# Performance work log

Measured on AMD Instinct MI355X. Metric: run time of the kernel, lower is better.

The kernel has to match this reference:

```python
import jax, jax.numpy as jnp
import numpy as np

B, S, DM = 2, 2048, 1024
H, D = 16, 64  # num_heads, head_dim
EPS = 1e-5


def setup_inputs() -> dict:
    key = jax.random.key(0)
    ks = jax.random.split(key, 5)
    sc = 1.0 / np.sqrt(DM)
    return {
        "x": jax.random.normal(ks[0], (B, S, DM), jnp.float32),
        "wq": jax.random.normal(ks[1], (DM, DM), jnp.float32) * sc,
        "bq": jnp.zeros((DM,), jnp.float32),
        "wk": jax.random.normal(ks[2], (DM, DM), jnp.float32) * sc,
        "bk": jnp.zeros((DM,), jnp.float32),
        "wv": jax.random.normal(ks[3], (DM, DM), jnp.float32) * sc,
        "bv": jnp.zeros((DM,), jnp.float32),
        "wo": jax.random.normal(ks[4], (DM, DM), jnp.float32) * sc,
        "bo": jnp.zeros((DM,), jnp.float32),
        "alpha": jnp.ones((1,), jnp.float32),
    }


def reference(x, wq, bq, wk, bk, wv, bv, wo, bo, alpha):
    b, s, _ = x.shape
    # QKV projections -> [B, S, H, D]
    q = (x @ wq + bq).reshape(b, s, H, D)
    k = (x @ wk + bk).reshape(b, s, H, D)
    v = (x @ wv + bv).reshape(b, s, H, D)
    # YAT scores: (Q.K)^2 / (||Q-K||^2 + eps)
    dot = jnp.einsum("bqhd,bkhd->bhqk", q, k)  # [B,H,S,S]
    qn = jnp.einsum("bqhd,bqhd->bhq", q, q)    # ||q||^2
    kn = jnp.einsum("bkhd,bkhd->bhk", k, k)    # ||k||^2
    dist2 = qn[..., :, None] + kn[..., None, :] - 2.0 * dot
    scores = (dot * dot) / (dist2 + EPS)
    # alpha scaling: (sqrt(D)/log(1+D))^alpha
    scale = (jnp.sqrt(jnp.float32(D)) / jnp.log1p(jnp.float32(D))) ** alpha[0]
    attn = jax.nn.softmax(scores * scale, axis=-1)
    out = jnp.einsum("bhqk,bkhd->bqhd", attn, v).reshape(b, s, H * D)
    return out @ wo + bo
```

## Files before the change

### kernel.cpp

```cpp
#include <hip/hip_runtime.h>
#include <hip/hip_bf16.h>
#include <math.h>

typedef __bf16 bf16;
typedef bf16 bf16x4 __attribute__((ext_vector_type(4)));
typedef bf16 bf16x8 __attribute__((ext_vector_type(8)));
typedef float floatx4 __attribute__((ext_vector_type(4)));

#define MFMA16(a, b, c) __builtin_amdgcn_mfma_f32_16x16x32_bf16(a, b, c, 0, 0, 0)

__device__ __forceinline__ void split2(float v, bf16& h, bf16& l) {
    h = (bf16)v;
    l = (bf16)(v - (float)h);
}

__device__ __forceinline__ void gload16(const bf16* g, bf16* l) {
    __builtin_amdgcn_global_load_lds(
        (const __attribute__((address_space(1))) void*)g,
        (__attribute__((address_space(3))) void*)l, 16, 0, 0);
}

__global__ void split_x(const float* __restrict__ x, bf16* __restrict__ xh,
                        bf16* __restrict__ xl) {
    const int i = (blockIdx.x * 256 + threadIdx.x) * 8;
    float4 a = *(const float4*)(x + i);
    float4 b = *(const float4*)(x + i + 4);
    bf16x8 oh, ol;
    float f[8] = {a.x, a.y, a.z, a.w, b.x, b.y, b.z, b.w};
#pragma unroll
    for (int j = 0; j < 8; j++) { bf16 h, l; split2(f[j], h, l); oh[j] = h; ol[j] = l; }
    *(bf16x8*)(xh + i) = oh;
    *(bf16x8*)(xl + i) = ol;
}

__global__ void transpose_w(const float* __restrict__ wq, const float* __restrict__ wk,
                            const float* __restrict__ wv, const float* __restrict__ wo,
                            bf16* __restrict__ wt_qkv_h, bf16* __restrict__ wt_qkv_l,
                            bf16* __restrict__ wt_o_h) {
    const int z = blockIdx.z;
    const float* src = (z == 0) ? wq : (z == 1) ? wk : (z == 2) ? wv : wo;
    bf16* dsth = (z < 3) ? (wt_qkv_h + (size_t)z * 1024 * 1024) : wt_o_h;
    bf16* dstl = (z < 3) ? (wt_qkv_l + (size_t)z * 1024 * 1024) : nullptr;
    __shared__ float tile[32][33];
    const int x0 = blockIdx.x * 32, y0 = blockIdx.y * 32;
    const int tx = threadIdx.x, ty = threadIdx.y;
    for (int i = 0; i < 32; i += 8)
        tile[ty + i][tx] = src[(size_t)(y0 + ty + i) * 1024 + x0 + tx];
    __syncthreads();
    for (int i = 0; i < 32; i += 8) {
        bf16 h, l;
        split2(tile[tx][ty + i], h, l);
        dsth[(size_t)(x0 + ty + i) * 1024 + y0 + tx] = h;
        if (dstl) dstl[(size_t)(x0 + ty + i) * 1024 + y0 + tx] = l;
    }
}

__global__ __launch_bounds__(256, 2) void gemm_qkv3(
    const bf16* __restrict__ Ah, const bf16* __restrict__ Al,
    const bf16* __restrict__ Bth, const bf16* __restrict__ Btl,
    const float* __restrict__ bq, const float* __restrict__ bk,
    const float* __restrict__ bv,
    bf16* __restrict__ Qh, bf16* __restrict__ Ql,
    bf16* __restrict__ Kh, bf16* __restrict__ Kl, bf16* __restrict__ VtG) {
    __shared__ bf16 Ash[128 * 32];
    __shared__ bf16 Asl[128 * 32];
    __shared__ bf16 Bsh[128 * 32];
    __shared__ bf16 Bsl[128 * 32];

    const int t = threadIdx.x;
    const int lane = t & 63, wave = t >> 6;
    const int quad = lane >> 4, l16 = lane & 15;
    const int m0 = blockIdx.x * 128, n0 = blockIdx.y * 128;
    const int wm = (wave >> 1) * 64, wn = (wave & 1) * 64;
    const bool full = (n0 < 2048);

    const int srow = wave * 16 + (lane >> 2);
    const int scol = (lane & 3) * 8;
    const bf16* gAh = Ah + (size_t)(m0 + srow) * 1024 + scol;
    const bf16* gAl = Al + (size_t)(m0 + srow) * 1024 + scol;
    const bf16* gBh = Bth + (size_t)(n0 + srow) * 1024 + scol;
    const bf16* gBl = Btl + (size_t)(n0 + srow) * 1024 + scol;
    bf16* lAh = &Ash[wave * 16 * 32];
    bf16* lAl = &Asl[wave * 16 * 32];
    bf16* lBh = &Bsh[wave * 16 * 32];
    bf16* lBl = &Bsl[wave * 16 * 32];

    floatx4 acc[4][4] = {};

    for (int k0 = 0; k0 < 1024; k0 += 32) {
        gload16(gAh + k0, lAh);
        gload16(gAh + 64 * 1024 + k0, lAh + 64 * 32);
        gload16(gBh + k0, lBh);
        gload16(gBh + 64 * 1024 + k0, lBh + 64 * 32);
        if (full) {
            gload16(gAl + k0, lAl);
            gload16(gAl + 64 * 1024 + k0, lAl + 64 * 32);
            gload16(gBl + k0, lBl);
            gload16(gBl + 64 * 1024 + k0, lBl + 64 * 32);
        }
        __syncthreads();
        bf16x8 afh[4], bfh[4];
#pragma unroll
        for (int i = 0; i < 4; i++)
            afh[i] = *(bf16x8*)&Ash[(wm + i * 16 + l16) * 32 + quad * 8];
#pragma unroll
        for (int j = 0; j < 4; j++)
            bfh[j] = *(bf16x8*)&Bsh[(wn + j * 16 + l16) * 32 + quad * 8];
        if (full) {
            bf16x8 afl[4], bfl[4];
#pragma unroll
            for (int i = 0; i < 4; i++)
                afl[i] = *(bf16x8*)&Asl[(wm + i * 16 + l16) * 32 + quad * 8];
#pragma unroll
            for (int j = 0; j < 4; j++)
                bfl[j] = *(bf16x8*)&Bsl[(wn + j * 16 + l16) * 32 + quad * 8];
#pragma unroll
            for (int i = 0; i < 4; i++)
#pragma unroll
                for (int j = 0; j < 4; j++) {
                    acc[i][j] = MFMA16(afh[i], bfh[j], acc[i][j]);
                    acc[i][j] = MFMA16(afh[i], bfl[j], acc[i][j]);
                    acc[i][j] = MFMA16(afl[i], bfh[j], acc[i][j]);
                }
        } else {
#pragma unroll
            for (int i = 0; i < 4; i++)
#pragma unroll
                for (int j = 0; j < 4; j++)
                    acc[i][j] = MFMA16(afh[i], bfh[j], acc[i][j]);
        }
        __syncthreads();
    }

    const int which = n0 >> 10;
    const float* bias = (which == 0) ? bq : (which == 1) ? bk : bv;
#pragma unroll
    for (int i = 0; i < 4; i++)
#pragma unroll
        for (int j = 0; j < 4; j++) {
            const int col = n0 + wn + j * 16 + l16;
            const int o = col & 1023;
            const int h = o >> 6, d = o & 63;
            const float bvv = bias[o];
            const int gm0 = m0 + wm + i * 16 + quad * 4;
            const int b = gm0 >> 11;
            if (which == 2) {
                bf16x4 pv;
#pragma unroll
                for (int r = 0; r < 4; r++) pv[r] = (bf16)(acc[i][j][r] + bvv);
                const int s0 = gm0 & 2047;
                *(bf16x4*)&VtG[((size_t)((b * 16 + h) * 64 + d)) * 2048 + s0] = pv;
            } else {
#pragma unroll
                for (int r = 0; r < 4; r++) {
                    const int gm = gm0 + r;
                    const int s = gm & 2047;
                    const size_t idx = (size_t)((b * 16 + h) * 2048 + s) * 64 + d;
                    const float val = acc[i][j][r] + bvv;
                    bf16 hi, lo;
                    split2(val, hi, lo);
                    if (which == 0) { Qh[idx] = hi; Ql[idx] = lo; }
                    else            { Kh[idx] = hi; Kl[idx] = lo; }
                }
            }
        }
}

__global__ void kn_kernel(const bf16* __restrict__ Kh, const bf16* __restrict__ Kl,
                          float* __restrict__ knG) {
    const int i = blockIdx.x * 256 + threadIdx.x;
    const bf16* ph = Kh + (size_t)i * 64;
    const bf16* pl = Kl + (size_t)i * 64;
    float s = 0.f;
#pragma unroll
    for (int d0 = 0; d0 < 64; d0 += 8) {
        bf16x8 vh = *(const bf16x8*)(ph + d0);
        bf16x8 vl = *(const bf16x8*)(pl + d0);
#pragma unroll
        for (int j = 0; j < 8; j++) { float x = (float)vh[j] + (float)vl[j]; s += x * x; }
    }
    knG[i] = s;
}

__global__ __launch_bounds__(256, 2) void attn_kernel(
    const bf16* __restrict__ Qh, const bf16* __restrict__ Ql,
    const bf16* __restrict__ Kh, const bf16* __restrict__ Kl,
    const bf16* __restrict__ VtG, const float* __restrict__ knG,
    bf16* __restrict__ O, const float* __restrict__ alphap) {
    __shared__ bf16 Ksh[64 * 72];
    __shared__ bf16 Ksl[64 * 72];
    __shared__ bf16 Vs[64 * 72];
    __shared__ bf16 Pt[4][32 * 72];
    __shared__ float knL[64];

    const int t = threadIdx.x, lane = t & 63, wave = t >> 6;
    const int quad = lane >> 4, l16 = lane & 15;
    const int bh = blockIdx.x;
    const int qw = blockIdx.y * 128 + wave * 32;

    const float alpha = alphap[0];
    const float C = powf(8.0f / log1pf(64.0f), alpha) * 1.44269504f;

    const size_t qrow0 = ((size_t)bh * 2048 + qw + l16) * 64;
    const size_t qrow1 = qrow0 + 16 * 64;
    bf16x8 bq0h[2], bq1h[2], bq0l[2], bq1l[2];
    bq0h[0] = *(const bf16x8*)(Qh + qrow0 + quad * 8);
    bq1h[0] = *(const bf16x8*)(Qh + qrow0 + 32 + quad * 8);
    bq0l[0] = *(const bf16x8*)(Ql + qrow0 + quad * 8);
    bq1l[0] = *(const bf16x8*)(Ql + qrow0 + 32 + quad * 8);
    bq0h[1] = *(const bf16x8*)(Qh + qrow1 + quad * 8);
    bq1h[1] = *(const bf16x8*)(Qh + qrow1 + 32 + quad * 8);
    bq0l[1] = *(const bf16x8*)(Ql + qrow1 + quad * 8);
    bq1l[1] = *(const bf16x8*)(Ql + qrow1 + 32 + quad * 8);

    float qne[2];
#pragma unroll
    for (int qg = 0; qg < 2; qg++) {
        float qn = 0.f;
#pragma unroll
        for (int j = 0; j < 8; j++) {
            float x0 = (float)bq0h[qg][j] + (float)bq0l[qg][j];
            float x1 = (float)bq1h[qg][j] + (float)bq1l[qg][j];
            qn += x0 * x0 + x1 * x1;
        }
        qn += __shfl_xor(qn, 16, 64);
        qn += __shfl_xor(qn, 32, 64);
        qne[qg] = qn + 1e-5f;
    }

    floatx4 acco[2][4] = {};
    float m_i[2] = {0.f, 0.f};
    float l_i[2] = {0.f, 0.f};

    const int srow = t >> 3;
    const int scol = (t & 7) * 8;
    const size_t vrow0 = ((size_t)bh * 64 + srow) * 2048;
    const size_t vrow1 = ((size_t)bh * 64 + srow + 32) * 2048;
    const float* knB = knG + (size_t)bh * 2048;

    for (int kc = 0; kc < 2048; kc += 64) {
        const size_t kbase = (size_t)(bh * 2048 + kc) * 64;
        bf16x8 kh0 = *(const bf16x8*)(Kh + kbase + srow * 64 + scol);
        bf16x8 kh1 = *(const bf16x8*)(Kh + kbase + (32 + srow) * 64 + scol);
        bf16x8 kl0 = *(const bf16x8*)(Kl + kbase + srow * 64 + scol);
        bf16x8 kl1 = *(const bf16x8*)(Kl + kbase + (32 + srow) * 64 + scol);
        bf16x8 v0 = *(const bf16x8*)(VtG + vrow0 + kc + scol);
        bf16x8 v1 = *(const bf16x8*)(VtG + vrow1 + kc + scol);
        __syncthreads();
        *(bf16x8*)&Ksh[srow * 72 + scol] = kh0;
        *(bf16x8*)&Ksh[(32 + srow) * 72 + scol] = kh1;
        *(bf16x8*)&Ksl[srow * 72 + scol] = kl0;
        *(bf16x8*)&Ksl[(32 + srow) * 72 + scol] = kl1;
        *(bf16x8*)&Vs[srow * 72 + scol] = v0;
        *(bf16x8*)&Vs[(32 + srow) * 72 + scol] = v1;
        if (t < 16) *(float4*)&knL[t * 4] = *(const float4*)(knB + kc + t * 4);
        __syncthreads();

        float pbuf[2][4][4];
        float mloc[2] = {0.f, 0.f};
#pragma unroll
        for (int sub = 0; sub < 4; sub++) {
            bf16x8 a0h = *(bf16x8*)&Ksh[(sub * 16 + l16) * 72 + quad * 8];
            bf16x8 a1h = *(bf16x8*)&Ksh[(sub * 16 + l16) * 72 + 32 + quad * 8];
            bf16x8 a0l = *(bf16x8*)&Ksl[(sub * 16 + l16) * 72 + quad * 8];
            bf16x8 a1l = *(bf16x8*)&Ksl[(sub * 16 + l16) * 72 + 32 + quad * 8];
            floatx4 ac0 = {}, ac1 = {};
            ac0 = MFMA16(a0h, bq0h[0], ac0);
            ac0 = MFMA16(a1h, bq1h[0], ac0);
            ac0 = MFMA16(a0h, bq0l[0], ac0);
            ac0 = MFMA16(a1h, bq1l[0], ac0);
            ac0 = MFMA16(a0l, bq0h[0], ac0);
            ac0 = MFMA16(a1l, bq1h[0], ac0);
            ac1 = MFMA16(a0h, bq0h[1], ac1);
            ac1 = MFMA16(a1h, bq1h[1], ac1);
            ac1 = MFMA16(a0h, bq0l[1], ac1);
            ac1 = MFMA16(a1h, bq1l[1], ac1);
            ac1 = MFMA16(a0l, bq0h[1], ac1);
            ac1 = MFMA16(a1l, bq1h[1], ac1);
            const floatx4 knv = *(const floatx4*)&knL[sub * 16 + quad * 4];
#pragma unroll
            for (int r = 0; r < 4; r++) {
                const float d0 = ac0[r];
                const float d1 = ac1[r];
                const float e0 = fmaf(-2.0f, d0, qne[0] + knv[r]);
                const float e1 = fmaf(-2.0f, d1, qne[1] + knv[r]);
                const float s0 = C * d0 * d0 * __builtin_amdgcn_rcpf(e0);
                const float s1 = C * d1 * d1 * __builtin_amdgcn_rcpf(e1);
                pbuf[0][sub][r] = s0;
                pbuf[1][sub][r] = s1;
                mloc[0] = fmaxf(mloc[0], s0);
                mloc[1] = fmaxf(mloc[1], s1);
            }
        }

        bf16* Pw = Pt[wave];
#pragma unroll
        for (int qg = 0; qg < 2; qg++) {
            float mx = mloc[qg];
            mx = fmaxf(mx, __shfl_xor(mx, 16, 64));
            mx = fmaxf(mx, __shfl_xor(mx, 32, 64));
            const float mnew = fmaxf(m_i[qg], mx);
            const float al = __builtin_amdgcn_exp2f(m_i[qg] - mnew);
            float rs = 0.f;
            bf16* Pq = Pw + (qg * 16 + l16) * 72;
#pragma unroll
            for (int sub = 0; sub < 4; sub++) {
                bf16x4 pv;
#pragma unroll
                for (int r = 0; r < 4; r++) {
                    const float p = __builtin_amdgcn_exp2f(pbuf[qg][sub][r] - mnew);
                    rs += p;
                    pv[r] = (bf16)p;
                }
                *(bf16x4*)&Pq[sub * 16 + quad * 4] = pv;
            }
            rs += __shfl_xor(rs, 16, 64);
            rs += __shfl_xor(rs, 32, 64);
            l_i[qg] = l_i[qg] * al + rs;
            m_i[qg] = mnew;
#pragma unroll
            for (int dsub = 0; dsub < 4; dsub++) acco[qg][dsub] *= al;
        }

        bf16x8 bp0[2], bp1[2];
#pragma unroll
        for (int qg = 0; qg < 2; qg++) {
            bp0[qg] = *(bf16x8*)&Pw[(qg * 16 + l16) * 72 + quad * 8];
            bp1[qg] = *(bf16x8*)&Pw[(qg * 16 + l16) * 72 + 32 + quad * 8];
        }
#pragma unroll
        for (int dsub = 0; dsub < 4; dsub++) {
            bf16x8 a0 = *(bf16x8*)&Vs[(dsub * 16 + l16) * 72 + quad * 8];
            bf16x8 a1 = *(bf16x8*)&Vs[(dsub * 16 + l16) * 72 + 32 + quad * 8];
            acco[0][dsub] = MFMA16(a0, bp0[0], acco[0][dsub]);
            acco[0][dsub] = MFMA16(a1, bp1[0], acco[0][dsub]);
            acco[1][dsub] = MFMA16(a0, bp0[1], acco[1][dsub]);
            acco[1][dsub] = MFMA16(a1, bp1[1], acco[1][dsub]);
        }
    }

    const int b = bh >> 4, h = bh & 15;
#pragma unroll
    for (int qg = 0; qg < 2; qg++) {
        const int s = qw + qg * 16 + l16;
        const float rl = 1.0f / l_i[qg];
        const size_t obase = (size_t)(b * 2048 + s) * 1024 + h * 64;
#pragma unroll
        for (int dsub = 0; dsub < 4; dsub++) {
            bf16x4 ov;
#pragma unroll
            for (int r = 0; r < 4; r++) ov[r] = (bf16)(acco[qg][dsub][r] * rl);
            *(bf16x4*)&O[obase + dsub * 16 + quad * 4] = ov;
        }
    }
}

__global__ __launch_bounds__(256, 2) void gemm_out(
    const bf16* __restrict__ A, const bf16* __restrict__ Bt,
    const float* __restrict__ bias, float* __restrict__ outC) {
    __shared__ bf16 As[128 * 32];
    __shared__ bf16 Bs[128 * 32];

    const int t = threadIdx.x;
    const int lane = t & 63, wave = t >> 6;
    const int quad = lane >> 4, l16 = lane & 15;
    const int m0 = blockIdx.x * 128, n0 = blockIdx.y * 128;
    const int wm = (wave >> 1) * 64, wn = (wave & 1) * 64;

    const int srow = wave * 16 + (lane >> 2);
    const int scol = (lane & 3) * 8;
    const bf16* gA0 = A + (size_t)(m0 + srow) * 1024 + scol;
    const bf16* gB0 = Bt + (size_t)(n0 + srow) * 1024 + scol;
    bf16* lA = &As[wave * 16 * 32];
    bf16* lB = &Bs[wave * 16 * 32];

    floatx4 acc[4][4] = {};

    for (int k0 = 0; k0 < 1024; k0 += 32) {
        gload16(gA0 + k0, lA);
        gload16(gA0 + 64 * 1024 + k0, lA + 64 * 32);
        gload16(gB0 + k0, lB);
        gload16(gB0 + 64 * 1024 + k0, lB + 64 * 32);
        __syncthreads();
        bf16x8 af[4], bf_[4];
#pragma unroll
        for (int i = 0; i < 4; i++)
            af[i] = *(bf16x8*)&As[(wm + i * 16 + l16) * 32 + quad * 8];
#pragma unroll
        for (int j = 0; j < 4; j++)
            bf_[j] = *(bf16x8*)&Bs[(wn + j * 16 + l16) * 32 + quad * 8];
#pragma unroll
        for (int i = 0; i < 4; i++)
#pragma unroll
            for (int j = 0; j < 4; j++)
                acc[i][j] = MFMA16(af[i], bf_[j], acc[i][j]);
        __syncthreads();
    }

#pragma unroll
    for (int i = 0; i < 4; i++)
#pragma unroll
        for (int j = 0; j < 4; j++) {
            const int col = n0 + wn + j * 16 + l16;
            const float bvv = bias[col];
#pragma unroll
            for (int r = 0; r < 4; r++) {
                const int gm = m0 + wm + i * 16 + quad * 4 + r;
                outC[(size_t)gm * 1024 + col] = acc[i][j][r] + bvv;
            }
        }
}

extern "C" void kernel_launch(void* const* d_in, const int* in_sizes, int n_in,
                              void* d_out, int out_size, void* d_ws, size_t ws_size,
                              hipStream_t stream) {
    const float* x  = (const float*)d_in[0];
    const float* wq = (const float*)d_in[1];
    const float* bq = (const float*)d_in[2];
    const float* wk = (const float*)d_in[3];
    const float* bk = (const float*)d_in[4];
    const float* wv = (const float*)d_in[5];
    const float* bv = (const float*)d_in[6];
    const float* wo = (const float*)d_in[7];
    const float* bo = (const float*)d_in[8];
    const float* alpha = (const float*)d_in[9];

    char* ws = (char*)d_ws;
    const size_t MB = 1024 * 1024;
    bf16* wqkv_h = (bf16*)(ws);
    bf16* wqkv_l = (bf16*)(ws + 6 * MB);
    bf16* wo_h   = (bf16*)(ws + 12 * MB);
    float* knG   = (float*)(ws + 14 * MB);
    bf16* x_h    = (bf16*)(ws + 16 * MB);
    bf16* x_l    = (bf16*)(ws + 24 * MB);
    bf16* Q_h    = (bf16*)(ws + 32 * MB);
    bf16* Q_l    = (bf16*)(ws + 40 * MB);
    bf16* K_h    = (bf16*)(ws + 48 * MB);
    bf16* K_l    = (bf16*)(ws + 56 * MB);
    bf16* Vt_g   = (bf16*)(ws + 64 * MB);
    bf16* Ob     = (bf16*)(ws);

    split_x<<<dim3(2048), 256, 0, stream>>>(x, x_h, x_l);
    transpose_w<<<dim3(32, 32, 4), dim3(32, 8), 0, stream>>>(
        wq, wk, wv, wo, wqkv_h, wqkv_l, wo_h);
    gemm_qkv3<<<dim3(32, 24), 256, 0, stream>>>(
        x_h, x_l, wqkv_h, wqkv_l, bq, bk, bv, Q_h, Q_l, K_h, K_l, Vt_g);
    kn_kernel<<<dim3(256), 256, 0, stream>>>(K_h, K_l, knG);
    attn_kernel<<<dim3(32, 16), 256, 0, stream>>>(
        Q_h, Q_l, K_h, K_l, Vt_g, knG, Ob, alpha);
    gemm_out<<<dim3(32, 8), 256, 0, stream>>>(Ob, wo_h, bo, (float*)d_out);
}
```

Measured before the change: 293.7 us.

## Double-buffer K/V tiles in LDS to overlap global loads with attention compute

The attention kernel's K-high, K-low, V and key-norm tiles in shared memory are now double-buffered. The next chunk's global loads are issued into registers before the current chunk is computed, then written to the other buffer afterwards. This cuts the loop from two barriers per iteration to one and hides global load latency behind the MFMA and softmax work. In exchange, shared memory use roughly doubles for those tiles and register pressure rises from holding prefetched data, which may affect occupancy at the 2-blocks-per-CU launch bound.

After: 293.1 us. About the same (-0.2%).

```diff
diff --git a/kernel.cpp b/kernel.cpp
--- a/kernel.cpp
+++ b/kernel.cpp
@@ -187,11 +187,11 @@
     const bf16* __restrict__ Kh, const bf16* __restrict__ Kl,
     const bf16* __restrict__ VtG, const float* __restrict__ knG,
     bf16* __restrict__ O, const float* __restrict__ alphap) {
-    __shared__ bf16 Ksh[64 * 72];
-    __shared__ bf16 Ksl[64 * 72];
-    __shared__ bf16 Vs[64 * 72];
+    __shared__ bf16 Ksh[2][64 * 72];
+    __shared__ bf16 Ksl[2][64 * 72];
+    __shared__ bf16 Vs[2][64 * 72];
     __shared__ bf16 Pt[4][32 * 72];
-    __shared__ float knL[64];
+    __shared__ float knL[2][64];
 
     const int t = threadIdx.x, lane = t & 63, wave = t >> 6;
     const int quad = lane >> 4, l16 = lane & 15;
@@ -238,32 +238,19 @@
     const size_t vrow1 = ((size_t)bh * 64 + srow + 32) * 2048;
     const float* knB = knG + (size_t)bh * 2048;
 
-    for (int kc = 0; kc < 2048; kc += 64) {
-        const size_t kbase = (size_t)(bh * 2048 + kc) * 64;
-        bf16x8 kh0 = *(const bf16x8*)(Kh + kbase + srow * 64 + scol);
-        bf16x8 kh1 = *(const bf16x8*)(Kh + kbase + (32 + srow) * 64 + scol);
-        bf16x8 kl0 = *(const bf16x8*)(Kl + kbase + srow * 64 + scol);
-        bf16x8 kl1 = *(const bf16x8*)(Kl + kbase + (32 + srow) * 64 + scol);
-        bf16x8 v0 = *(const bf16x8*)(VtG + vrow0 + kc + scol);
-        bf16x8 v1 = *(const bf16x8*)(VtG + vrow1 + kc + scol);
-        __syncthreads();
-        *(bf16x8*)&Ksh[srow * 72 + scol] = kh0;
-        *(bf16x8*)&Ksh[(32 + srow) * 72 + scol] = kh1;
-        *(bf16x8*)&Ksl[srow * 72 + scol] = kl0;
-        *(bf16x8*)&Ksl[(32 + srow) * 72 + scol] = kl1;
-        *(bf16x8*)&Vs[srow * 72 + scol] = v0;
-        *(bf16x8*)&Vs[(32 + srow) * 72 + scol] = v1;
-        if (t < 16) *(float4*)&knL[t * 4] = *(const float4*)(knB + kc + t * 4);
-        __syncthreads();
-
+    auto do_chunk = [&](int ib) {
+        const bf16* KshC = Ksh[ib];
+        const bf16* KslC = Ksl[ib];
+        const bf16* VsC = Vs[ib];
+        const float* knC = knL[ib];
         float pbuf[2][4][4];
         float mloc[2] = {0.f, 0.f};
 #pragma unroll
         for (int sub = 0; sub < 4; sub++) {
-            bf16x8 a0h = *(bf16x8*)&Ksh[(sub * 16 + l16) * 72 + quad * 8];
-            bf16x8 a1h = *(bf16x8*)&Ksh[(sub * 16 + l16) * 72 + 32 + quad * 8];
-            bf16x8 a0l = *(bf16x8*)&Ksl[(sub * 16 + l16) * 72 + quad * 8];
-            bf16x8 a1l = *(bf16x8*)&Ksl[(sub * 16 + l16) * 72 + 32 + quad * 8];
+            bf16x8 a0h = *(bf16x8*)&KshC[(sub * 16 + l16) * 72 + quad * 8];
+            bf16x8 a1h = *(bf16x8*)&KshC[(sub * 16 + l16) * 72 + 32 + quad * 8];
+            bf16x8 a0l = *(bf16x8*)&KslC[(sub * 16 + l16) * 72 + quad * 8];
+            bf16x8 a1l = *(bf16x8*)&KslC[(sub * 16 + l16) * 72 + 32 + quad * 8];
             floatx4 ac0 = {}, ac1 = {};
             ac0 = MFMA16(a0h, bq0h[0], ac0);
             ac0 = MFMA16(a1h, bq1h[0], ac0);
@@ -277,7 +264,7 @@
             ac1 = MFMA16(a1h, bq1l[1], ac1);
             ac1 = MFMA16(a0l, bq0h[1], ac1);
             ac1 = MFMA16(a1l, bq1h[1], ac1);
-            const floatx4 knv = *(const floatx4*)&knL[sub * 16 + quad * 4];
+            const floatx4 knv = *(const floatx4*)&knC[sub * 16 + quad * 4];
 #pragma unroll
             for (int r = 0; r < 4; r++) {
                 const float d0 = ac0[r];
@@ -292,7 +279,6 @@
                 mloc[1] = fmaxf(mloc[1], s1);
             }
         }
-
         bf16* Pw = Pt[wave];
 #pragma unroll
         for (int qg = 0; qg < 2; qg++) {
@@ -321,7 +307,6 @@
 #pragma unroll
             for (int dsub = 0; dsub < 4; dsub++) acco[qg][dsub] *= al;
         }
-
         bf16x8 bp0[2], bp1[2];
 #pragma unroll
         for (int qg = 0; qg < 2; qg++) {
@@ -330,14 +315,58 @@
         }
 #pragma unroll
         for (int dsub = 0; dsub < 4; dsub++) {
-            bf16x8 a0 = *(bf16x8*)&Vs[(dsub * 16 + l16) * 72 + quad * 8];
-            bf16x8 a1 = *(bf16x8*)&Vs[(dsub * 16 + l16) * 72 + 32 + quad * 8];
+            bf16x8 a0 = *(bf16x8*)&VsC[(dsub * 16 + l16) * 72 + quad * 8];
+            bf16x8 a1 = *(bf16x8*)&VsC[(dsub * 16 + l16) * 72 + 32 + quad * 8];
             acco[0][dsub] = MFMA16(a0, bp0[0], acco[0][dsub]);
             acco[0][dsub] = MFMA16(a1, bp1[0], acco[0][dsub]);
             acco[1][dsub] = MFMA16(a0, bp0[1], acco[1][dsub]);
             acco[1][dsub] = MFMA16(a1, bp1[1], acco[1][dsub]);
         }
-    }
+    };
+
+    {
+        const size_t kb = (size_t)(bh * 2048) * 64;
+        bf16x8 k0 = *(const bf16x8*)(Kh + kb + srow * 64 + scol);
+        bf16x8 k1 = *(const bf16x8*)(Kh + kb + (32 + srow) * 64 + scol);
+        bf16x8 c0 = *(const bf16x8*)(Kl + kb + srow * 64 + scol);
+        bf16x8 c1 = *(const bf16x8*)(Kl + kb + (32 + srow) * 64 + scol);
+        bf16x8 v0 = *(const bf16x8*)(VtG + vrow0 + scol);
+        bf16x8 v1 = *(const bf16x8*)(VtG + vrow1 + scol);
+        *(bf16x8*)&Ksh[0][srow * 72 + scol] = k0;
+        *(bf16x8*)&Ksh[0][(32 + srow) * 72 + scol] = k1;
+        *(bf16x8*)&Ksl[0][srow * 72 + scol] = c0;
+        *(bf16x8*)&Ksl[0][(32 + srow) * 72 + scol] = c1;
+        *(bf16x8*)&Vs[0][srow * 72 + scol] = v0;
+        *(bf16x8*)&Vs[0][(32 + srow) * 72 + scol] = v1;
+        if (t < 16) *(float4*)&knL[0][t * 4] = *(const float4*)(knB + t * 4);
+    }
+    __syncthreads();
+
+    for (int ic = 0; ic < 31; ic++) {
+        const int cur = ic & 1, nxt = cur ^ 1;
+        const int kc = (ic + 1) * 64;
+        const size_t kb = (size_t)(bh * 2048 + kc) * 64;
+        bf16x8 nk0 = *(const bf16x8*)(Kh + kb + srow * 64 + scol);
+        bf16x8 nk1 = *(const bf16x8*)(Kh + kb + (32 + srow) * 64 + scol);
+        bf16x8 nc0 = *(const bf16x8*)(Kl + kb + srow * 64 + scol);
+        bf16x8 nc1 = *(const bf16x8*)(Kl + kb + (32 + srow) * 64 + scol);
+        bf16x8 nv0 = *(const bf16x8*)(VtG + vrow0 + kc + scol);
+        bf16x8 nv1 = *(const bf16x8*)(VtG + vrow1 + kc + scol);
+        float4 nkn;
+        if (t < 16) nkn = *(const float4*)(knB + kc + t * 4);
+
+        do_chunk(cur);
+
+        *(bf16x8*)&Ksh[nxt][srow * 72 + scol] = nk0;
+        *(bf16x8*)&Ksh[nxt][(32 + srow) * 72 + scol] = nk1;
+        *(bf16x8*)&Ksl[nxt][srow * 72 + scol] = nc0;
+        *(bf16x8*)&Ksl[nxt][(32 + srow) * 72 + scol] = nc1;
+        *(bf16x8*)&Vs[nxt][srow * 72 + scol] = nv0;
+        *(bf16x8*)&Vs[nxt][(32 + srow) * 72 + scol] = nv1;
+        if (t < 16) *(float4*)&knL[nxt][t * 4] = nkn;
+        __syncthreads();
+    }
+    do_chunk(1);
 
     const int b = bh >> 4, h = bh & 15;
 #pragma unroll
```
